# Performance work log

Hardware: AMD Instinct MI355X
Metric: run time of the kernel (lower is better)

## Reference

```python
import jax, jax.numpy as jnp
import numpy as np

N, C, H, W = 2, 128, 64, 256
GROUPS, S = 8, 9  # 3x3 search window


def setup_inputs() -> dict:
    key = jax.random.key(0)
    k1, k2, k3 = jax.random.split(key, 3)
    left = jax.random.normal(k1, (N, C, H, W), jnp.float32)
    right = jax.random.normal(k2, (N, C, H, W), jnp.float32)
    # per-pixel learned offsets: (N, S*2, H, W), reshaped to (N,S,2,H,W) inside
    extra_offset = jax.random.normal(k3, (N, S * 2, H, W), jnp.float32)
    return {"left_feature": left, "right_feature": right, "extra_offset": extra_offset}


def _bilinear_sample(im, x, y):
    """im: (N,C,H,W); x,y: (N,L) pixel coords. Zero padding outside borders
    (matches bilinear_grid_sample: 1-px zero pad + index clamp into pad)."""
    n, c, h, w = im.shape
    x0f = jnp.floor(x)
    y0f = jnp.floor(y)
    x1f = x0f + 1.0
    y1f = y0f + 1.0
    wa = (x1f - x) * (y1f - y)
    wb = (x1f - x) * (y - y0f)
    wc = (x - x0f) * (y1f - y)
    wd = (x - x0f) * (y - y0f)
    ph, pw = h + 2, w + 2
    im_p = jnp.pad(im, ((0, 0), (0, 0), (1, 1), (1, 1))).reshape(n, c, ph * pw)
    x0 = jnp.clip(x0f.astype(jnp.int32) + 1, 0, pw - 1)
    x1 = jnp.clip(x1f.astype(jnp.int32) + 1, 0, pw - 1)
    y0 = jnp.clip(y0f.astype(jnp.int32) + 1, 0, ph - 1)
    y1 = jnp.clip(y1f.astype(jnp.int32) + 1, 0, ph - 1)

    def g(xi, yi):
        idx = (xi + yi * pw)[:, None, :]  # (N,1,L) -> broadcast over C
        return jnp.take_along_axis(im_p, idx, axis=2)

    out = (g(x0, y0) * wa[:, None, :] + g(x0, y1) * wb[:, None, :]
           + g(x1, y0) * wc[:, None, :] + g(x1, y1) * wd[:, None, :])
    return out  # (N,C,L)


def reference(left_feature, right_feature, extra_offset):
    n, c, h, w = left_feature.shape
    cg = c // GROUPS
    # base 3x3 offsets, (x,y) pairs in torch meshgrid 'ij' order
    r = jnp.arange(-1, 2, dtype=jnp.float32)
    xg, yg = jnp.meshgrid(r, r, indexing='ij')
    base = jnp.stack([xg, yg], axis=-1).reshape(S, 2)  # (9,2)
    eo = extra_offset.reshape(n, S, 2, h, w).transpose(0, 1, 3, 4, 2)  # (N,S,H,W,2)
    off = base[None, :, None, None, :] + eo
    gx = jnp.arange(w, dtype=jnp.float32)
    gy = jnp.arange(h, dtype=jnp.float32)
    x = (off[..., 0] + gx[None, None, None, :]).reshape(n, -1)  # (N, S*H*W)
    y = (off[..., 1] + gy[None, None, :, None]).reshape(n, -1)
    # offsets are shared across groups -> sample all channels once
    sampled = _bilinear_sample(right_feature, x, y).reshape(n, GROUPS, cg, S, h, w)
    left_g = left_feature.reshape(n, GROUPS, cg, 1, h, w)
    corr = jnp.mean(left_g * sampled, axis=2)  # (N, GROUPS, S, H, W)
    return corr.reshape(n, GROUPS * S, h, w)
```

## Files before the change

kernel.cpp:

```cpp
#include <hip/hip_runtime.h>
#include <stdint.h>


#define NB 2
#define CC 128
#define HH 64
#define WW 256
#define GG 8
#define CG 16
#define SS 9
#define HW (HH * WW)
#define TY 4
#define RW 5
#define NSLOT 16
#define SLOTDW 288
#define B0 4
#define PLANEDW (NSLOT * SLOTDW)
#define NPAIR 8
#define SMEMDW (NPAIR * PLANEDW)

typedef __fp16 h2v __attribute__((ext_vector_type(2)));

static __device__ __forceinline__ uint32_t pkrtz(float a, float b) {
    h2v v = __builtin_amdgcn_cvt_pkrtz(a, b);
    return __builtin_bit_cast(uint32_t, v);
}
static __device__ __forceinline__ h2v u2h(uint32_t u) {
    return __builtin_bit_cast(h2v, u);
}

#if __has_builtin(__builtin_amdgcn_fdot2)
#define FDOT2(A, B, C) __builtin_amdgcn_fdot2((A), (B), (C), false)
#else
#define FDOT2(A, B, C) fmaf((float)(A).x, (float)(B).x, \
                            fmaf((float)(A).y, (float)(B).y, (C)))
#endif

__global__ __launch_bounds__(1024) void corr_kernel(
    const float* __restrict__ left, const float* __restrict__ right,
    const float* __restrict__ eo, float* __restrict__ out)
{
    __shared__ uint32_t smem[SMEMDW];

    const int tid = threadIdx.x;
    const int lane = tid & 63;
    const int wv = tid >> 6;
    const int bid = blockIdx.x;
    const int g = bid & (GG - 1);
    const int h0 = ((bid >> 3) & 15) << 2;
    const int n = bid >> 7;
    const int gch = g * CG;

    const int virt_row0 = h0 - RW;
    const int row0 = max(0, virt_row0);
    const int row_last = min(HH - 1, h0 + TY + RW - 1);
    const int nrows = row_last - row0 + 1;
    const int sbase = row0 - virt_row0 + 1;

    const int hh = tid >> 8;
    const int h = h0 + hh;
    const int wcol = tid & 255;
    const int pix = h * WW + wcol;

    const float* rnb = right + (size_t)n * CC * HW;
    const float* lp  = left  + (size_t)(n * CC + gch) * HW + pix;
    const float* eob = eo + (size_t)n * SS * 2 * HW + pix;

    for (int i = tid; i < SMEMDW / 4; i += 1024)
        *(uint4*)&smem[4 * i] = make_uint4(0u, 0u, 0u, 0u);
    __syncthreads();

#pragma unroll
    for (int p = 0; p < NPAIR; ++p) {
        if (wv < nrows) {
            const float* s0 = rnb + (size_t)(gch + 2 * p) * HW
                            + (row0 + wv) * WW + 4 * lane;
            const float4 a = *(const float4*)s0;
            const float4 b = *(const float4*)(s0 + HW);
            uint4 o;
            o.x = pkrtz(a.x, b.x);
            o.y = pkrtz(a.y, b.y);
            o.z = pkrtz(a.z, b.z);
            o.w = pkrtz(a.w, b.w);
            *(uint4*)&smem[p * PLANEDW + (sbase + wv) * SLOTDW + B0 + 4 * lane] = o;
        }
    }

    uint32_t lvpk[NPAIR];
#pragma unroll
    for (int p = 0; p < NPAIR; ++p)
        lvpk[p] = pkrtz(lp[(size_t)(2 * p) * HW], lp[(size_t)(2 * p + 1) * HW]);

    __syncthreads();

    float acc[SS];
#pragma unroll
    for (int s = 0; s < SS; ++s) acc[s] = 0.0f;

    const char* sb = (const char*)smem;

#pragma unroll
    for (int s = 0; s < SS; ++s) {
        const float x = (float)(s / 3 - 1) + eob[(2 * s) * HW] + (float)wcol;
        const float y = (float)(s % 3 - 1) + eob[(2 * s + 1) * HW] + (float)h;
        const float x0f = floorf(x), y0f = floorf(y);
        const float fx0 = x - x0f, fx1 = 1.0f - fx0;
        const float fy0 = y - y0f, fy1 = 1.0f - fy0;
        const int x0 = (int)x0f, y0 = (int)y0f;
        const int x1 = x0 + 1,   y1 = y0 + 1;
        const bool vx0 = (unsigned)x0 < (unsigned)WW;
        const bool vx1 = (unsigned)x1 < (unsigned)WW;
        const bool vy0 = (unsigned)y0 < (unsigned)HH;
        const bool vy1 = (unsigned)y1 < (unsigned)HH;
        const float wA = (vx0 && vy0) ? fx1 * fy1 : 0.0f;
        const float wB = (vx1 && vy0) ? fx0 * fy1 : 0.0f;
        const float wC = (vx0 && vy1) ? fx1 * fy0 : 0.0f;
        const float wD = (vx1 && vy1) ? fx0 * fy0 : 0.0f;

        const bool bad = (vy0 && (y0 < row0 || y0 > row_last)) ||
                         (vy1 && (y1 < row0 || y1 > row_last));

        if (__builtin_expect(!bad, 1)) {
            const int xc = min(max(x0, -1), WW);
            const int rr = min(max(y0 - virt_row0 + 1, 0), NSLOT - 2);
            const char* base = sb + (size_t)((rr * SLOTDW + B0 + xc) * 4);
#pragma unroll
            for (int p = 0; p < NPAIR; ++p) {
                const char* bp = base + p * (PLANEDW * 4);
                const h2v A  = *(const h2v*)(bp);
                const h2v Bv = *(const h2v*)(bp + 4);
                const h2v Cv = *(const h2v*)(bp + SLOTDW * 4);
                const h2v Dv = *(const h2v*)(bp + SLOTDW * 4 + 4);
                const h2v lv = u2h(lvpk[p]);
                float t =    wA * FDOT2(A,  lv, 0.0f);
                t = fmaf(wB, FDOT2(Bv, lv, 0.0f), t);
                t = fmaf(wC, FDOT2(Cv, lv, 0.0f), t);
                t = fmaf(wD, FDOT2(Dv, lv, 0.0f), t);
                acc[s] += t;
            }
        } else {
            const int cx0 = min(max(x0, 0), WW - 1), cx1 = min(max(x1, 0), WW - 1);
            const int cy0 = min(max(y0, 0), HH - 1), cy1 = min(max(y1, 0), HH - 1);
#pragma unroll
            for (int p = 0; p < NPAIR; ++p) {
                const h2v lv = u2h(lvpk[p]);
#pragma unroll
                for (int c2 = 0; c2 < 2; ++c2) {
                    const float* rp2 = rnb + (size_t)(gch + 2 * p + c2) * HW;
                    const float v = wA * rp2[cy0 * WW + cx0] + wB * rp2[cy0 * WW + cx1]
                                  + wC * rp2[cy1 * WW + cx0] + wD * rp2[cy1 * WW + cx1];
                    acc[s] += (c2 ? (float)lv.y : (float)lv.x) * v;
                }
            }
        }
    }

    float* ob = out + ((size_t)(n * GG + g) * SS) * HW + pix;
#pragma unroll
    for (int s = 0; s < SS; ++s)
        ob[s * HW] = acc[s] * (1.0f / CG);
}

extern "C" void kernel_launch(void* const* d_in, const int* in_sizes, int n_in,
                              void* d_out, int out_size, void* d_ws, size_t ws_size,
                              hipStream_t stream) {
    const float* left  = (const float*)d_in[0];
    const float* right = (const float*)d_in[1];
    const float* eo    = (const float*)d_in[2];
    float* out = (float*)d_out;
    (void)d_ws; (void)ws_size; (void)in_sizes; (void)n_in; (void)out_size;

    dim3 grid(NB * (HH / TY) * GG);
    dim3 block(1024);
    corr_kernel<<<grid, block, 0, stream>>>(left, right, eo, out);
}
```

Measured before the change: 25.45 us.

## Pack four channels per LDS slot for 128-bit bilinear neighbor reads

Reorganizes the shared-memory staging of right-feature rows so each pixel column stores four fp16 channels (two packed dwords) contiguously, with adjacent x-neighbors interleaved. The hot bilinear path can then fetch both horizontal neighbors for four channels with a single 128-bit LDS read per row, instead of four 32-bit reads per channel pair. This cuts the number of LDS instructions and address computations in the inner loop. It also changes the staging writes to two 128-bit stores per lane and slightly grows the padded row stride.

After: 45.55 us. 1.79x slower.

```diff
diff --git a/kernel.cpp b/kernel.cpp
--- a/kernel.cpp
+++ b/kernel.cpp
@@ -13,11 +13,11 @@
 #define TY 4
 #define RW 5
 #define NSLOT 16
-#define SLOTDW 288
-#define B0 4
-#define PLANEDW (NSLOT * SLOTDW)
-#define NPAIR 8
-#define SMEMDW (NPAIR * PLANEDW)
+#define SLOTQW 544
+#define B0 2
+#define PLANEQW (NSLOT * SLOTQW)
+#define NQUAD 4
+#define SMEMDW (NQUAD * PLANEQW)
 
 typedef __fp16 h2v __attribute__((ext_vector_type(2)));
 
@@ -71,25 +71,34 @@
     __syncthreads();
 
 #pragma unroll
-    for (int p = 0; p < NPAIR; ++p) {
+    for (int q = 0; q < NQUAD; ++q) {
         if (wv < nrows) {
-            const float* s0 = rnb + (size_t)(gch + 2 * p) * HW
+            const float* s0 = rnb + (size_t)(gch + 4 * q) * HW
                             + (row0 + wv) * WW + 4 * lane;
             const float4 a = *(const float4*)s0;
             const float4 b = *(const float4*)(s0 + HW);
-            uint4 o;
-            o.x = pkrtz(a.x, b.x);
-            o.y = pkrtz(a.y, b.y);
-            o.z = pkrtz(a.z, b.z);
-            o.w = pkrtz(a.w, b.w);
-            *(uint4*)&smem[p * PLANEDW + (sbase + wv) * SLOTDW + B0 + 4 * lane] = o;
+            const float4 c = *(const float4*)(s0 + 2 * HW);
+            const float4 d = *(const float4*)(s0 + 3 * HW);
+            uint32_t* dst = &smem[q * PLANEQW + (sbase + wv) * SLOTQW
+                                  + B0 + 8 * lane];
+            uint4 o0, o1;
+            o0.x = pkrtz(a.x, b.x); o0.y = pkrtz(c.x, d.x);
+            o0.z = pkrtz(a.y, b.y); o0.w = pkrtz(c.y, d.y);
+            o1.x = pkrtz(a.z, b.z); o1.y = pkrtz(c.z, d.z);
+            o1.z = pkrtz(a.w, b.w); o1.w = pkrtz(c.w, d.w);
+            *(uint4*)dst = o0;
+            *(uint4*)(dst + 4) = o1;
         }
     }
 
-    uint32_t lvpk[NPAIR];
+    uint32_t lvq[2 * NQUAD];
 #pragma unroll
-    for (int p = 0; p < NPAIR; ++p)
-        lvpk[p] = pkrtz(lp[(size_t)(2 * p) * HW], lp[(size_t)(2 * p + 1) * HW]);
+    for (int q = 0; q < NQUAD; ++q) {
+        lvq[2 * q]     = pkrtz(lp[(size_t)(4 * q) * HW],
+                               lp[(size_t)(4 * q + 1) * HW]);
+        lvq[2 * q + 1] = pkrtz(lp[(size_t)(4 * q + 2) * HW],
+                               lp[(size_t)(4 * q + 3) * HW]);
+    }
 
     __syncthreads();
 
@@ -123,33 +132,34 @@
         if (__builtin_expect(!bad, 1)) {
             const int xc = min(max(x0, -1), WW);
             const int rr = min(max(y0 - virt_row0 + 1, 0), NSLOT - 2);
-            const char* base = sb + (size_t)((rr * SLOTDW + B0 + xc) * 4);
+            const char* base = sb + (size_t)((rr * SLOTQW + B0 + 2 * xc) * 4);
+            float t = 0.0f;
 #pragma unroll
-            for (int p = 0; p < NPAIR; ++p) {
-                const char* bp = base + p * (PLANEDW * 4);
-                const h2v A  = *(const h2v*)(bp);
-                const h2v Bv = *(const h2v*)(bp + 4);
-                const h2v Cv = *(const h2v*)(bp + SLOTDW * 4);
-                const h2v Dv = *(const h2v*)(bp + SLOTDW * 4 + 4);
-                const h2v lv = u2h(lvpk[p]);
-                float t =    wA * FDOT2(A,  lv, 0.0f);
-                t = fmaf(wB, FDOT2(Bv, lv, 0.0f), t);
-                t = fmaf(wC, FDOT2(Cv, lv, 0.0f), t);
-                t = fmaf(wD, FDOT2(Dv, lv, 0.0f), t);
-                acc[s] += t;
+            for (int q = 0; q < NQUAD; ++q) {
+                const char* bp = base + q * (PLANEQW * 4);
+                const uint4 r0 = *(const uint4*)(bp);
+                const uint4 r1 = *(const uint4*)(bp + SLOTQW * 4);
+                const h2v lv0 = u2h(lvq[2 * q]), lv1 = u2h(lvq[2 * q + 1]);
+                t = fmaf(wA, FDOT2(u2h(r0.x), lv0, FDOT2(u2h(r0.y), lv1, 0.0f)), t);
+                t = fmaf(wB, FDOT2(u2h(r0.z), lv0, FDOT2(u2h(r0.w), lv1, 0.0f)), t);
+                t = fmaf(wC, FDOT2(u2h(r1.x), lv0, FDOT2(u2h(r1.y), lv1, 0.0f)), t);
+                t = fmaf(wD, FDOT2(u2h(r1.z), lv0, FDOT2(u2h(r1.w), lv1, 0.0f)), t);
             }
+            acc[s] += t;
         } else {
             const int cx0 = min(max(x0, 0), WW - 1), cx1 = min(max(x1, 0), WW - 1);
             const int cy0 = min(max(y0, 0), HH - 1), cy1 = min(max(y1, 0), HH - 1);
 #pragma unroll
-            for (int p = 0; p < NPAIR; ++p) {
-                const h2v lv = u2h(lvpk[p]);
+            for (int q = 0; q < NQUAD; ++q) {
+                const h2v lv0 = u2h(lvq[2 * q]), lv1 = u2h(lvq[2 * q + 1]);
 #pragma unroll
-                for (int c2 = 0; c2 < 2; ++c2) {
-                    const float* rp2 = rnb + (size_t)(gch + 2 * p + c2) * HW;
+                for (int c2 = 0; c2 < 4; ++c2) {
+                    const float* rp2 = rnb + (size_t)(gch + 4 * q + c2) * HW;
                     const float v = wA * rp2[cy0 * WW + cx0] + wB * rp2[cy0 * WW + cx1]
                                   + wC * rp2[cy1 * WW + cx0] + wD * rp2[cy1 * WW + cx1];
-                    acc[s] += (c2 ? (float)lv.y : (float)lv.x) * v;
+                    const float lvc = (c2 == 0) ? (float)lv0.x : (c2 == 1) ? (float)lv0.y
+                                    : (c2 == 2) ? (float)lv1.x : (float)lv1.y;
+                    acc[s] += lvc * v;
                 }
             }
         }
```

## Interleave channels per pixel in LDS to enable 128-bit vector loads

Applied to the files above, without the earlier changes.

Changes the shared-memory layout from channel-pair planes to a pixel-major layout where each pixel stores its 16 half-precision channels in two 16-byte halves. The bilinear tap reads become two uint4 LDS loads per corner instead of eight scattered dword loads, and the weight multiply is hoisted out of the channel loop. Staging now does scalar strided global loads per channel instead of float4 loads, which may coalesce less well, and the 16-byte LDS reads at arbitrary pixel offsets may cause bank conflicts.

New measurement: 21.14 us. -16.9%, faster.

```diff
diff --git a/kernel.cpp b/kernel.cpp
--- a/kernel.cpp
+++ b/kernel.cpp
@@ -13,11 +13,9 @@
 #define TY 4
 #define RW 5
 #define NSLOT 16
-#define SLOTDW 288
-#define B0 4
-#define PLANEDW (NSLOT * SLOTDW)
-#define NPAIR 8
-#define SMEMDW (NPAIR * PLANEDW)
+#define HALFDW 1056
+#define SLOTQ (2 * HALFDW)
+#define SMEMDW (NSLOT * SLOTQ)
 
 typedef __fp16 h2v __attribute__((ext_vector_type(2)));
 
@@ -35,6 +33,20 @@
 #define FDOT2(A, B, C) fmaf((float)(A).x, (float)(B).x, \
                             fmaf((float)(A).y, (float)(B).y, (C)))
 #endif
+
+#define DOT16(LOP, RES)                                                        \
+  {                                                                            \
+    const uint4 u0_ = *(const uint4*)(LOP);                                    \
+    const uint4 u1_ = *(const uint4*)((LOP) + HALFDW);                         \
+    RES = FDOT2(u2h(u0_.x), u2h(lvpk[0]),                                      \
+          FDOT2(u2h(u0_.y), u2h(lvpk[1]),                                      \
+          FDOT2(u2h(u0_.z), u2h(lvpk[2]),                                      \
+          FDOT2(u2h(u0_.w), u2h(lvpk[3]),                                      \
+          FDOT2(u2h(u1_.x), u2h(lvpk[4]),                                      \
+          FDOT2(u2h(u1_.y), u2h(lvpk[5]),                                      \
+          FDOT2(u2h(u1_.z), u2h(lvpk[6]),                                      \
+          FDOT2(u2h(u1_.w), u2h(lvpk[7]), 0.0f))))))));                        \
+  }
 
 __global__ __launch_bounds__(1024) void corr_kernel(
     const float* __restrict__ left, const float* __restrict__ right,
@@ -71,24 +83,24 @@
     __syncthreads();
 
 #pragma unroll
-    for (int p = 0; p < NPAIR; ++p) {
+    for (int pass = 0; pass < 4; ++pass) {
         if (wv < nrows) {
-            const float* s0 = rnb + (size_t)(gch + 2 * p) * HW
-                            + (row0 + wv) * WW + 4 * lane;
-            const float4 a = *(const float4*)s0;
-            const float4 b = *(const float4*)(s0 + HW);
-            uint4 o;
-            o.x = pkrtz(a.x, b.x);
-            o.y = pkrtz(a.y, b.y);
-            o.z = pkrtz(a.z, b.z);
-            o.w = pkrtz(a.w, b.w);
-            *(uint4*)&smem[p * PLANEDW + (sbase + wv) * SLOTDW + B0 + 4 * lane] = o;
+            const int cq = 64 * pass + lane;
+            const float* s0 = rnb + (size_t)gch * HW + (row0 + wv) * WW + cq;
+            uint32_t pk8[8];
+#pragma unroll
+            for (int p = 0; p < 8; ++p)
+                pk8[p] = pkrtz(s0[(size_t)(2 * p) * HW],
+                               s0[(size_t)(2 * p + 1) * HW]);
+            uint32_t* dst = &smem[(sbase + wv) * SLOTQ + 4 * (cq + 1)];
+            *(uint4*)dst            = make_uint4(pk8[0], pk8[1], pk8[2], pk8[3]);
+            *(uint4*)(dst + HALFDW) = make_uint4(pk8[4], pk8[5], pk8[6], pk8[7]);
         }
     }
 
-    uint32_t lvpk[NPAIR];
+    uint32_t lvpk[8];
 #pragma unroll
-    for (int p = 0; p < NPAIR; ++p)
+    for (int p = 0; p < 8; ++p)
         lvpk[p] = pkrtz(lp[(size_t)(2 * p) * HW], lp[(size_t)(2 * p + 1) * HW]);
 
     __syncthreads();
@@ -96,8 +108,6 @@
     float acc[SS];
 #pragma unroll
     for (int s = 0; s < SS; ++s) acc[s] = 0.0f;
-
-    const char* sb = (const char*)smem;
 
 #pragma unroll
     for (int s = 0; s < SS; ++s) {
@@ -123,26 +133,19 @@
         if (__builtin_expect(!bad, 1)) {
             const int xc = min(max(x0, -1), WW);
             const int rr = min(max(y0 - virt_row0 + 1, 0), NSLOT - 2);
-            const char* base = sb + (size_t)((rr * SLOTDW + B0 + xc) * 4);
-#pragma unroll
-            for (int p = 0; p < NPAIR; ++p) {
-                const char* bp = base + p * (PLANEDW * 4);
-                const h2v A  = *(const h2v*)(bp);
-                const h2v Bv = *(const h2v*)(bp + 4);
-                const h2v Cv = *(const h2v*)(bp + SLOTDW * 4);
-                const h2v Dv = *(const h2v*)(bp + SLOTDW * 4 + 4);
-                const h2v lv = u2h(lvpk[p]);
-                float t =    wA * FDOT2(A,  lv, 0.0f);
-                t = fmaf(wB, FDOT2(Bv, lv, 0.0f), t);
-                t = fmaf(wC, FDOT2(Cv, lv, 0.0f), t);
-                t = fmaf(wD, FDOT2(Dv, lv, 0.0f), t);
-                acc[s] += t;
-            }
+            const uint32_t* rp0 = smem + rr * SLOTQ + 4 * (xc + 1);
+            const uint32_t* rp1 = rp0 + SLOTQ;
+            float dA, dB, dC, dD;
+            DOT16(rp0,     dA)
+            DOT16(rp0 + 4, dB)
+            DOT16(rp1,     dC)
+            DOT16(rp1 + 4, dD)
+            acc[s] += fmaf(wA, dA, fmaf(wB, dB, fmaf(wC, dC, wD * dD)));
         } else {
             const int cx0 = min(max(x0, 0), WW - 1), cx1 = min(max(x1, 0), WW - 1);
             const int cy0 = min(max(y0, 0), HH - 1), cy1 = min(max(y1, 0), HH - 1);
 #pragma unroll
-            for (int p = 0; p < NPAIR; ++p) {
+            for (int p = 0; p < 8; ++p) {
                 const h2v lv = u2h(lvpk[p]);
 #pragma unroll
                 for (int c2 = 0; c2 < 2; ++c2) {
```
